# Optimization experiments

Hardware: AMD Instinct MI355X
Metric: run time of the kernel (lower is better)

## Reference

```python
import jax, jax.numpy as jnp
import numpy as np

M = 24  # lpc_order (even -> kernel_p=[-1,1], kernel_q=[1,1], no padding)


def _roots_to_poly_real(r):
    """Monic polynomial coefficients prod_k (x - r_k), real part.
    r: (..., N) complex -> (..., N+1) real coefficients (descending powers).
    Sequential recursion c <- c - r_k * shift(c), matching RootsToPolynomial.
    """
    N = r.shape[-1]
    c0 = jnp.zeros(r.shape[:-1] + (N + 1,), dtype=r.dtype).at[..., 0].set(1.0)

    def step(c, root):
        shifted = jnp.concatenate([jnp.zeros_like(c[..., :1]), c[..., :-1]], axis=-1)
        return c - root[..., None] * shifted, None

    c, _ = jax.lax.scan(step, c0, jnp.moveaxis(r, -1, 0))  # scan over the N roots
    return c.real


def setup_inputs() -> dict:
    key = jax.random.key(0)
    # LSP frequencies in (0, pi); uniform [0,1) is a valid subset. Index 0 is gain K.
    w = jax.random.uniform(key, (16, 65536, M + 1), dtype=jnp.float32)
    return {"w": w}


def reference(w):
    K, wf = w[..., :1], w[..., 1:]            # gain, M LSP frequencies
    z = jnp.exp(1j * wf)                       # complex64 unit-circle roots
    p = z[..., 1::2]                           # M/2 roots
    q = z[..., 0::2]                           # M/2 roots (M even)
    # Pair each root with its conjugate -> real polynomials of degree M
    P = _roots_to_poly_real(jnp.concatenate([p, jnp.conj(p)], axis=-1))  # (..., M+1)
    Q = _roots_to_poly_real(jnp.concatenate([q, jnp.conj(q)], axis=-1))  # (..., M+1)
    # conv1d with kernel_p=[-1,1] (cross-correlation): out[i] = P[i+1]-P[i]
    pc = P[..., 1:] - P[..., :-1]              # (..., M)
    # conv1d with kernel_q=[1,1]: out[i] = Q[i]+Q[i+1]
    qc = Q[..., 1:] + Q[..., :-1]              # (..., M)
    a = 0.5 * (pc + qc)
    return jnp.concatenate([K, a], axis=-1)    # (..., M+1)
```

## Files before the change

kernel.cpp:

```cpp
#include <hip/hip_runtime.h>

#define RW 25
#define RPB 256

typedef float f4 __attribute__((ext_vector_type(4)));
typedef float f2 __attribute__((ext_vector_type(2)));

__global__ __launch_bounds__(256) void lsp2lpc_kernel(const float* __restrict__ in,
                                                      float* __restrict__ out) {
    __shared__ float sm[RPB * RW];
    const long long row0 = (long long)blockIdx.x * RPB;
    const f4* gin4  = (const f4*)(in  + row0 * RW);
    f4*       gout4 = (f4*)(out + row0 * RW);
    f4*       sm4   = (f4*)sm;
    const int tid = threadIdx.x;

    #pragma unroll
    for (int i = 0; i < 6; ++i)
        sm4[tid + i * 256] = gin4[tid + i * 256];
    if (tid < 64)
        sm4[tid + 1536] = gin4[tid + 1536];
    __syncthreads();

    const float* wr = &sm[tid * RW];
    const float K = wr[0];

    f2 c[12];
    #pragma unroll
    for (int k = 0; k < 12; ++k) {
        c[k].x = -2.f * __cosf(wr[2 + 2 * k]);
        c[k].y = -2.f * __cosf(wr[1 + 2 * k]);
    }

    f2 PQ[RW];
    #pragma unroll
    for (int j = 0; j < RW; ++j) PQ[j] = (f2)(0.f);
    PQ[0] = (f2)(1.f);

    #pragma unroll
    for (int k = 0; k < 12; ++k) {
        const f2 a = c[k];
        #pragma unroll
        for (int j = 2 * k + 2; j >= 2; --j)
            PQ[j] = PQ[j] + a * PQ[j - 1] + PQ[j - 2];
        PQ[1] = PQ[1] + a * PQ[0];
    }

    float* orow = &sm[tid * RW];
    orow[0] = K;
    #pragma unroll
    for (int i = 0; i < 24; ++i)
        orow[1 + i] = 0.5f * ((PQ[i + 1].x - PQ[i].x) + (PQ[i + 1].y + PQ[i].y));
    __syncthreads();

    #pragma unroll
    for (int i = 0; i < 6; ++i)
        __builtin_nontemporal_store(sm4[tid + i * 256], &gout4[tid + i * 256]);
    if (tid < 64)
        __builtin_nontemporal_store(sm4[tid + 1536], &gout4[tid + 1536]);
}

extern "C" void kernel_launch(void* const* d_in, const int* in_sizes, int n_in,
                              void* d_out, int out_size, void* d_ws, size_t ws_size,
                              hipStream_t stream) {
    const float* in = (const float*)d_in[0];
    float* out = (float*)d_out;
    const int nrows = in_sizes[0] / RW;
    const int nblocks = nrows / RPB;
    lsp2lpc_kernel<<<nblocks, RPB, 0, stream>>>(in, out);
}
```

Measured before the change: 38.03 us.

## Process four tiles per block with register prefetch of the next tile

Each block now loops over four 256-row tiles and prefetches the next tile's input into registers while computing the current one, so global loads overlap with the polynomial computation. The launch shrinks by four times and gains a minimum-occupancy hint. Output stores become ordinary stores instead of nontemporal ones. The change adds an extra barrier per tile and extra register pressure, and leaves fewer blocks to hide memory latency.

```diff
diff --git a/kernel.cpp b/kernel.cpp
--- a/kernel.cpp
+++ b/kernel.cpp
@@ -2,62 +2,77 @@
 
 #define RW 25
 #define RPB 256
+#define TPB 4
 
 typedef float f4 __attribute__((ext_vector_type(4)));
 typedef float f2 __attribute__((ext_vector_type(2)));
 
-__global__ __launch_bounds__(256) void lsp2lpc_kernel(const float* __restrict__ in,
-                                                      float* __restrict__ out) {
+__global__ __launch_bounds__(256, 4) void lsp2lpc_kernel(const float* __restrict__ in,
+                                                         float* __restrict__ out) {
     __shared__ float sm[RPB * RW];
-    const long long row0 = (long long)blockIdx.x * RPB;
-    const f4* gin4  = (const f4*)(in  + row0 * RW);
-    f4*       gout4 = (f4*)(out + row0 * RW);
-    f4*       sm4   = (f4*)sm;
+    f4* sm4 = (f4*)sm;
     const int tid = threadIdx.x;
+    const long long tile0 = (long long)blockIdx.x * TPB;
 
-    #pragma unroll
-    for (int i = 0; i < 6; ++i)
-        sm4[tid + i * 256] = gin4[tid + i * 256];
-    if (tid < 64)
-        sm4[tid + 1536] = gin4[tid + 1536];
-    __syncthreads();
-
-    const float* wr = &sm[tid * RW];
-    const float K = wr[0];
-
-    f2 c[12];
-    #pragma unroll
-    for (int k = 0; k < 12; ++k) {
-        c[k].x = -2.f * __cosf(wr[2 + 2 * k]);
-        c[k].y = -2.f * __cosf(wr[1 + 2 * k]);
+    f4 r0, r1, r2, r3, r4, r5, r6;
+    {
+        const f4* g = (const f4*)(in + tile0 * (RPB * RW));
+        r0 = g[tid];        r1 = g[tid + 256];  r2 = g[tid + 512];
+        r3 = g[tid + 768];  r4 = g[tid + 1024]; r5 = g[tid + 1280];
+        if (tid < 64) r6 = g[tid + 1536];
     }
 
-    f2 PQ[RW];
-    #pragma unroll
-    for (int j = 0; j < RW; ++j) PQ[j] = (f2)(0.f);
-    PQ[0] = (f2)(1.f);
+    for (int t = 0; t < TPB; ++t) {
+        sm4[tid] = r0;        sm4[tid + 256] = r1;  sm4[tid + 512] = r2;
+        sm4[tid + 768] = r3;  sm4[tid + 1024] = r4; sm4[tid + 1280] = r5;
+        if (tid < 64) sm4[tid + 1536] = r6;
+        __syncthreads();
 
-    #pragma unroll
-    for (int k = 0; k < 12; ++k) {
-        const f2 a = c[k];
+        if (t + 1 < TPB) {
+            const f4* g = (const f4*)(in + (tile0 + t + 1) * (RPB * RW));
+            r0 = g[tid];        r1 = g[tid + 256];  r2 = g[tid + 512];
+            r3 = g[tid + 768];  r4 = g[tid + 1024]; r5 = g[tid + 1280];
+            if (tid < 64) r6 = g[tid + 1536];
+        }
+
+        const float* wr = &sm[tid * RW];
+        const float K = wr[0];
+
+        f2 c[12];
         #pragma unroll
-        for (int j = 2 * k + 2; j >= 2; --j)
-            PQ[j] = PQ[j] + a * PQ[j - 1] + PQ[j - 2];
-        PQ[1] = PQ[1] + a * PQ[0];
+        for (int k = 0; k < 12; ++k) {
+            c[k].x = -2.f * __cosf(wr[2 + 2 * k]);
+            c[k].y = -2.f * __cosf(wr[1 + 2 * k]);
+        }
+
+        f2 PQ[RW];
+        #pragma unroll
+        for (int j = 0; j < RW; ++j) PQ[j] = (f2)(0.f);
+        PQ[0] = (f2)(1.f);
+
+        #pragma unroll
+        for (int k = 0; k < 12; ++k) {
+            const f2 a = c[k];
+            #pragma unroll
+            for (int j = 2 * k + 2; j >= 2; --j)
+                PQ[j] = PQ[j] + a * PQ[j - 1] + PQ[j - 2];
+            PQ[1] = PQ[1] + a * PQ[0];
+        }
+
+        float* orow = &sm[tid * RW];
+        orow[0] = K;
+        #pragma unroll
+        for (int i = 0; i < 24; ++i)
+            orow[1 + i] = 0.5f * ((PQ[i + 1].x - PQ[i].x) + (PQ[i + 1].y + PQ[i].y));
+        __syncthreads();
+
+        f4* go = (f4*)(out + (tile0 + t) * (RPB * RW));
+        go[tid] = sm4[tid];               go[tid + 256] = sm4[tid + 256];
+        go[tid + 512] = sm4[tid + 512];   go[tid + 768] = sm4[tid + 768];
+        go[tid + 1024] = sm4[tid + 1024]; go[tid + 1280] = sm4[tid + 1280];
+        if (tid < 64) go[tid + 1536] = sm4[tid + 1536];
+        __syncthreads();
     }
-
-    float* orow = &sm[tid * RW];
-    orow[0] = K;
-    #pragma unroll
-    for (int i = 0; i < 24; ++i)
-        orow[1 + i] = 0.5f * ((PQ[i + 1].x - PQ[i].x) + (PQ[i + 1].y + PQ[i].y));
-    __syncthreads();
-
-    #pragma unroll
-    for (int i = 0; i < 6; ++i)
-        __builtin_nontemporal_store(sm4[tid + i * 256], &gout4[tid + i * 256]);
-    if (tid < 64)
-        __builtin_nontemporal_store(sm4[tid + 1536], &gout4[tid + 1536]);
 }
 
 extern "C" void kernel_launch(void* const* d_in, const int* in_sizes, int n_in,
@@ -66,6 +81,6 @@
     const float* in = (const float*)d_in[0];
     float* out = (float*)d_out;
     const int nrows = in_sizes[0] / RW;
-    const int nblocks = nrows / RPB;
+    const int nblocks = nrows / (RPB * TPB);
     lsp2lpc_kernel<<<nblocks, RPB, 0, stream>>>(in, out);
 }
```

After: 38.15 us. No clear change (+0.3%).
